# Kernel optimization log

Measured on AMD Instinct MI355X. Metric: run time of the kernel, lower is better.

The kernel has to match this reference:

```python
import jax, jax.numpy as jnp
import numpy as np


def setup_inputs() -> dict:
    key = jax.random.key(0)
    ks = jax.random.split(key, 5)
    B, C, T, Hh, Ww = 4, 64, 8, 32, 32
    HID = 32
    s = 0.05  # weight scale for numerically sane softmax logits
    return {
        "H": jax.random.normal(ks[0], (B, C, T, Hh, Ww), dtype=jnp.float32),
        "h": jax.random.normal(ks[1], (B, C, Hh, Ww), dtype=jnp.float32),
        "w_q": jax.random.normal(ks[2], (HID, C), dtype=jnp.float32) * s,
        "w_kv": jax.random.normal(ks[3], (HID, C), dtype=jnp.float32) * s,
        "w_o": jax.random.normal(ks[4], (C, HID), dtype=jnp.float32) * s,
    }


def reference(H, h, w_q, w_kv, w_o):
    B, C, T, Hh, Ww = H.shape
    N = Hh * Ww
    Hf = H.reshape(B, C, T, N)
    # 1x1 convs are pure channel-mixing matmuls
    H_kv = jnp.einsum('dc,bctn->bdtn', w_kv, Hf)                # [B, hid, T, N]
    h_q = jnp.einsum('dc,bchw->bdhw', w_q, h).reshape(B, -1, N)  # [B, hid, N]
    h_q = h_q.transpose(0, 2, 1)                                 # [B, N, hid]
    # per-timestep scores, vectorized over t: [B, T, N, N]
    a = jnp.einsum('bnd,bdtm->btnm', h_q, H_kv)
    # remove the diagonal of each per-timestep [N, N] block
    diag = jnp.einsum('btnn->btn', a)                            # [B, T, N]
    eye = jnp.eye(N, dtype=a.dtype)
    a = a - diag[..., :, None] * eye
    # concat over t along rows, softmax over the (T*N) row axis
    att = jax.nn.softmax(a.reshape(B, T * N, N), axis=1)         # [B, T*N, N]
    h_v = jnp.einsum('bdk,bkm->bdm', H_kv.reshape(B, -1, T * N), att)  # [B, hid, N]
    h_v = jnp.einsum('cd,bdhw->bchw', w_o, h_v.reshape(B, -1, Hh, Ww))
    return (h + h_v, att)
```

## Files before the change

### kernel.cpp

```cpp
#include <hip/hip_runtime.h>

typedef short bf16x8 __attribute__((ext_vector_type(8)));
typedef float f32x4  __attribute__((ext_vector_type(4)));
typedef unsigned short ushort_t;

#define HID 32
#define CC  64
#define TT  8
#define NN  1024
#define BB  4
#define KTOT 8192

__device__ __forceinline__ ushort_t f2b(float x) {
    unsigned int u = __float_as_uint(x);
    return (ushort_t)((u + 0x7fffu + ((u >> 16) & 1u)) >> 16);
}
__device__ __forceinline__ float b2f(ushort_t u) {
    return __uint_as_float((unsigned int)u << 16);
}

__global__ __launch_bounds__(256) void k_pre(const float* __restrict__ H,
                                             const float* __restrict__ h,
                                             const float* __restrict__ wq,
                                             const float* __restrict__ wkv,
                                             ushort_t* __restrict__ hqHI,
                                             ushort_t* __restrict__ hqLO,
                                             ushort_t* __restrict__ hkTH0,
                                             ushort_t* __restrict__ hkTH1,
                                             ushort_t* __restrict__ hkTL0,
                                             ushort_t* __restrict__ hkTL1,
                                             ushort_t* __restrict__ hkDB) {
    int bx = blockIdx.x;
    if (bx < 256) {
        int gid = bx * 256 + threadIdx.x;
        int dg = gid >> 15;
        int rest = gid & 32767;
        int b = rest >> 13, tn = rest & 8191;
        int d0 = dg << 4;
        float acc[16];
#pragma unroll
        for (int d = 0; d < 16; d++) acc[d] = 0.f;
        const float* Hb = H + (size_t)(b * CC) * KTOT + tn;
        const float* wb = wkv + d0 * CC;
#pragma unroll 8
        for (int c = 0; c < CC; c++) {
            float v = Hb[(size_t)c * KTOT];
#pragma unroll
            for (int d = 0; d < 16; d++) acc[d] += wb[d * CC + c] * v;
        }
        ushort_t thi[16], tlo[16];
#pragma unroll
        for (int d = 0; d < 16; d++) {
            ushort_t hi = f2b(acc[d]);
            thi[d] = hi;
            tlo[d] = f2b(acc[d] - b2f(hi));
        }
        size_t po = ((size_t)b * KTOT + tn) * 16;
        bf16x8* ohi = (bf16x8*)((dg ? hkTH1 : hkTH0) + po);
        bf16x8* olo = (bf16x8*)((dg ? hkTL1 : hkTL0) + po);
#pragma unroll
        for (int v8 = 0; v8 < 2; v8++) {
            bf16x8 a, l;
#pragma unroll
            for (int j = 0; j < 8; j++) { a[j] = (short)thi[v8*8+j]; l[j] = (short)tlo[v8*8+j]; }
            ohi[v8] = a; olo[v8] = l;
        }
#pragma unroll
        for (int d = 0; d < 16; d++)
            hkDB[((size_t)(b * HID) + d0 + d) * KTOT + tn] = thi[d];
    } else {
        int gid = (bx - 256) * 256 + threadIdx.x;
        int b = gid >> 10;
        float acc[HID];
#pragma unroll
        for (int d = 0; d < HID; d++) acc[d] = 0.f;
        const float* hb = h + (size_t)(b * CC) * NN + (gid & 1023);
#pragma unroll 4
        for (int c = 0; c < CC; c++) {
            float v = hb[c * NN];
#pragma unroll
            for (int d = 0; d < HID; d++) acc[d] += wq[d * CC + c] * v;
        }
        bf16x8* ohi = (bf16x8*)(hqHI + (size_t)gid * HID);
        bf16x8* olo = (bf16x8*)(hqLO + (size_t)gid * HID);
#pragma unroll
        for (int v8 = 0; v8 < 4; v8++) {
            bf16x8 thi, tlo;
#pragma unroll
            for (int j = 0; j < 8; j++) {
                float x = acc[v8 * 8 + j];
                ushort_t hi = f2b(x);
                thi[j] = (short)hi;
                tlo[j] = (short)f2b(x - b2f(hi));
            }
            ohi[v8] = thi; olo[v8] = tlo;
        }
    }
}

__global__ __launch_bounds__(1024) void k_fuse(const ushort_t* __restrict__ hqHI,
                                               const ushort_t* __restrict__ hqLO,
                                               const ushort_t* __restrict__ hkTH0,
                                               const ushort_t* __restrict__ hkTH1,
                                               const ushort_t* __restrict__ hkTL0,
                                               const ushort_t* __restrict__ hkTL1,
                                               const ushort_t* __restrict__ hkDB,
                                               const float* __restrict__ h,
                                               const float* __restrict__ wo,
                                               float* __restrict__ att,
                                               float* __restrict__ out0) {
    int bx = blockIdx.x;
    int logical = ((bx & 7) << 5) | (bx >> 3);
    int b = logical >> 6, mt = logical & 63;
    int mb = mt << 4;
    int tid = threadIdx.x;
    int wave = tid >> 6, lane = tid & 63;
    int g = lane >> 4, c = lane & 15;
    int t = wave >> 1;
    int nh = (wave & 1) << 9;

    __shared__ float csred[16][16];
    __shared__ float hvred[16][16][32];
    __shared__ float hvL[16][33];
    __shared__ __align__(16) ushort_t PT[16][16][40];

    size_t ako = ((size_t)b * KTOT + t * NN + (mb + c)) * 16 + (g & 1) * 8;
    bf16x8 akh = *(const bf16x8*)(((g >> 1) ? hkTH1 : hkTH0) + ako);
    bf16x8 akl = *(const bf16x8*)(((g >> 1) ? hkTL1 : hkTL0) + ako);

    const ushort_t* qhi = hqHI + ((size_t)(b << 10)) * HID;
    const ushort_t* qlo = hqLO + ((size_t)(b << 10)) * HID;
    const ushort_t* vb0 = hkDB + (size_t)(b * HID + c) * KTOT;
    const ushort_t* vb1 = hkDB + (size_t)(b * HID + 16 + c) * KTOT;
    ushort_t (*pt)[40] = PT[wave];

    f32x4 cs = {0.f, 0.f, 0.f, 0.f};
    f32x4 acc0 = {0.f,0.f,0.f,0.f}, acc1 = {0.f,0.f,0.f,0.f};
    for (int ks = 0; ks < 16; ks++) {
        int k0 = t * NN + nh + ks * 32;
#pragma unroll
        for (int half = 0; half < 2; half++) {
            int nb = nh + ks * 32 + half * 16;
            size_t qo = (size_t)(nb + c) * HID + 8 * g;
            bf16x8 qh = *(const bf16x8*)(qhi + qo);
            f32x4 sv = __builtin_amdgcn_mfma_f32_16x16x32_bf16(akh, qh, (f32x4){0.f,0.f,0.f,0.f}, 0, 0, 0);
            int n = nb + c;
            float e0 = __expf((n == mb + 4 * g + 0) ? 0.f : sv[0]);
            float e1 = __expf((n == mb + 4 * g + 1) ? 0.f : sv[1]);
            float e2 = __expf((n == mb + 4 * g + 2) ? 0.f : sv[2]);
            float e3 = __expf((n == mb + 4 * g + 3) ? 0.f : sv[3]);
            cs[0] += e0; cs[1] += e1; cs[2] += e2; cs[3] += e3;
            int kl = half * 16 + c;
            pt[4 * g + 0][kl] = f2b(e0);
            pt[4 * g + 1][kl] = f2b(e1);
            pt[4 * g + 2][kl] = f2b(e2);
            pt[4 * g + 3][kl] = f2b(e3);
        }
        bf16x8 pa = *(const bf16x8*)&pt[c][8 * g];
        bf16x8 v0 = *(const bf16x8*)(vb0 + k0 + 8 * g);
        bf16x8 v1 = *(const bf16x8*)(vb1 + k0 + 8 * g);
        acc0 = __builtin_amdgcn_mfma_f32_16x16x32_bf16(pa, v0, acc0, 0, 0, 0);
        acc1 = __builtin_amdgcn_mfma_f32_16x16x32_bf16(pa, v1, acc1, 0, 0, 0);
    }
#pragma unroll
    for (int off = 1; off <= 8; off <<= 1) {
        cs[0] += __shfl_xor(cs[0], off, 64);
        cs[1] += __shfl_xor(cs[1], off, 64);
        cs[2] += __shfl_xor(cs[2], off, 64);
        cs[3] += __shfl_xor(cs[3], off, 64);
    }
    if (c == 0) *(f32x4*)&csred[wave][4 * g] = cs;
    __syncthreads();
    f32x4 gs = {0.f, 0.f, 0.f, 0.f};
#pragma unroll
    for (int w = 0; w < 16; w++)
        gs += *(const f32x4*)&csred[w][4 * g];
    f32x4 vinv;
#pragma unroll
    for (int r = 0; r < 4; r++) vinv[r] = 1.0f / gs[r];

#pragma unroll
    for (int r = 0; r < 4; r++) {
        hvred[wave][4 * g + r][c]      = acc0[r] * vinv[r];
        hvred[wave][4 * g + r][16 + c] = acc1[r] * vinv[r];
    }

    float* attb = att + (size_t)b * KTOT * NN;
#pragma unroll 2
    for (int hs = 0; hs < 32; hs++) {
        int nb = nh + hs * 16;
        size_t qo = (size_t)(nb + c) * HID + 8 * g;
        bf16x8 qh = *(const bf16x8*)(qhi + qo);
        bf16x8 ql = *(const bf16x8*)(qlo + qo);
        f32x4 sv = __builtin_amdgcn_mfma_f32_16x16x32_bf16(akh, ql, (f32x4){0.f,0.f,0.f,0.f}, 0, 0, 0);
        sv = __builtin_amdgcn_mfma_f32_16x16x32_bf16(akl, qh, sv, 0, 0, 0);
        sv = __builtin_amdgcn_mfma_f32_16x16x32_bf16(akh, qh, sv, 0, 0, 0);
        int n = nb + c;
        f32x4 ev;
        ev[0] = __expf((n == mb + 4 * g + 0) ? 0.f : sv[0]) * vinv[0];
        ev[1] = __expf((n == mb + 4 * g + 1) ? 0.f : sv[1]) * vinv[1];
        ev[2] = __expf((n == mb + 4 * g + 2) ? 0.f : sv[2]) * vinv[2];
        ev[3] = __expf((n == mb + 4 * g + 3) ? 0.f : sv[3]) * vinv[3];
        *(f32x4*)(attb + (size_t)(t * NN + n) * NN + mb + 4 * g) = ev;
    }

    __syncthreads();
    if (tid < 512) {
        int m = tid >> 5, d = tid & 31;
        float s = 0.f;
#pragma unroll
        for (int w = 0; w < 16; w++) s += hvred[w][m][d];
        hvL[m][d] = s;
    }
    __syncthreads();
    {
        int cc = tid >> 4, mm = tid & 15;
        float v = h[(size_t)(b * CC + cc) * NN + mb + mm];
#pragma unroll
        for (int d = 0; d < HID; d++) v += wo[cc * HID + d] * hvL[mm][d];
        out0[(size_t)(b * CC + cc) * NN + mb + mm] = v;
    }
}

extern "C" void kernel_launch(void* const* d_in, const int* in_sizes, int n_in,
                              void* d_out, int out_size, void* d_ws, size_t ws_size,
                              hipStream_t stream) {
    const float* H   = (const float*)d_in[0];
    const float* h   = (const float*)d_in[1];
    const float* wq  = (const float*)d_in[2];
    const float* wkv = (const float*)d_in[3];
    const float* wo  = (const float*)d_in[4];

    float* out0 = (float*)d_out;
    float* att  = out0 + (size_t)BB * CC * NN;

    ushort_t* hqHI  = (ushort_t*)d_ws;
    ushort_t* hqLO  = hqHI  + 131072;
    ushort_t* hkTH0 = hqLO  + 131072;
    ushort_t* hkTH1 = hkTH0 + 524288;
    ushort_t* hkTL0 = hkTH1 + 524288;
    ushort_t* hkTL1 = hkTL0 + 524288;
    ushort_t* hkDB  = hkTL1 + 524288;

    k_pre <<<272, 256,  0, stream>>>(H, h, wq, wkv, hqHI, hqLO,
                                     hkTH0, hkTH1, hkTL0, hkTL1, hkDB);
    k_fuse<<<256, 1024, 0, stream>>>(hqHI, hqLO, hkTH0, hkTH1, hkTL0, hkTL1, hkDB,
                                     h, wo, att, out0);
}
```

Measured before the change: 85.10 us.

## Precompute softmax column sums in a separate kernel and fuse attention writes into main pass

Adds a k_psum kernel that computes partial softmax denominators over 32 K-chunks using the bf16-hi scores, so k_main can derive the normalizers up front. The main kernel then computes the exact 3-MFMA scores once, writing normalized attention and feeding the PV product in a single pass instead of two passes over N. This removes the recomputation of scores and the block-wide barrier before the attention write, at the cost of an extra launch and a separate sum pass. The normalizer now comes from hi-only scores while the numerators use the split-precision scores, so the rows may not sum exactly to one.

Result: no change. 85.62 us (+0.6%).

```diff
diff --git a/kernel.cpp b/kernel.cpp
--- a/kernel.cpp
+++ b/kernel.cpp
@@ -10,6 +10,8 @@
 #define NN  1024
 #define BB  4
 #define KTOT 8192
+#define NKC_P 32
+#define KCHUNK_P (KTOT/NKC_P)
 
 __device__ __forceinline__ ushort_t f2b(float x) {
     unsigned int u = __float_as_uint(x);
@@ -98,13 +100,56 @@
     }
 }
 
-__global__ __launch_bounds__(1024) void k_fuse(const ushort_t* __restrict__ hqHI,
+__global__ __launch_bounds__(512, 8) void k_psum(const ushort_t* __restrict__ hqHI,
+                                                 const ushort_t* __restrict__ hkTH0,
+                                                 const ushort_t* __restrict__ hkTH1,
+                                                 float* __restrict__ psum) {
+    int bx = blockIdx.x;
+    int b = bx >> 8, mt = (bx >> 5) & 7, kc = bx & 31;
+    int wave = threadIdx.x >> 6, lane = threadIdx.x & 63;
+    int g = lane >> 4, c = lane & 15;
+    int m = mt * 128 + wave * 16 + c;
+    int t = kc >> 2;
+    int nb0 = (kc & 3) << 8;
+
+    size_t bqo = ((size_t)b * KTOT + t * NN + m) * 16 + (g & 1) * 8;
+    bf16x8 bqh = *(const bf16x8*)(((g >> 1) ? hkTH1 : hkTH0) + bqo);
+
+    const ushort_t* qhi = hqHI + ((size_t)(b << 10)) * HID;
+
+    float csum0 = 0.f, csum1 = 0.f;
+    for (int s16 = 0; s16 < KCHUNK_P / 16; s16 += 2) {
+        int nbA = nb0 + s16 * 16;
+        int nbB = nbA + 16;
+        bf16x8 ahA = *(const bf16x8*)(qhi + (size_t)(nbA + c) * HID + 8 * g);
+        bf16x8 ahB = *(const bf16x8*)(qhi + (size_t)(nbB + c) * HID + 8 * g);
+        f32x4 svA = __builtin_amdgcn_mfma_f32_16x16x32_bf16(ahA, bqh, (f32x4){0.f,0.f,0.f,0.f}, 0, 0, 0);
+        f32x4 svB = __builtin_amdgcn_mfma_f32_16x16x32_bf16(ahB, bqh, (f32x4){0.f,0.f,0.f,0.f}, 0, 0, 0);
+        int nrowA = nbA + 4 * g;
+        int nrowB = nbB + 4 * g;
+#pragma unroll
+        for (int r = 0; r < 4; r++) {
+            float xA = (nrowA + r == m) ? 0.f : svA[r];
+            float xB = (nrowB + r == m) ? 0.f : svB[r];
+            csum0 += __expf(xA);
+            csum1 += __expf(xB);
+        }
+    }
+    float csum = csum0 + csum1;
+    csum += __shfl_xor(csum, 16);
+    csum += __shfl_xor(csum, 32);
+    if (lane < 16)
+        psum[(((size_t)(b * NKC_P + kc)) << 10) + mt * 128 + wave * 16 + lane] = csum;
+}
+
+__global__ __launch_bounds__(1024) void k_main(const ushort_t* __restrict__ hqHI,
                                                const ushort_t* __restrict__ hqLO,
                                                const ushort_t* __restrict__ hkTH0,
                                                const ushort_t* __restrict__ hkTH1,
                                                const ushort_t* __restrict__ hkTL0,
                                                const ushort_t* __restrict__ hkTL1,
                                                const ushort_t* __restrict__ hkDB,
+                                               const float* __restrict__ psum,
                                                const float* __restrict__ h,
                                                const float* __restrict__ wo,
                                                float* __restrict__ att,
@@ -119,10 +164,17 @@
     int t = wave >> 1;
     int nh = (wave & 1) << 9;
 
-    __shared__ float csred[16][16];
     __shared__ float hvred[16][16][32];
     __shared__ float hvL[16][33];
     __shared__ __align__(16) ushort_t PT[16][16][40];
+
+    f32x4 gs = {0.f, 0.f, 0.f, 0.f};
+#pragma unroll
+    for (int j = 0; j < NKC_P; j++)
+        gs += *(const f32x4*)(psum + (((size_t)(b * NKC_P + j)) << 10) + mb + 4 * g);
+    f32x4 vinv;
+#pragma unroll
+    for (int r = 0; r < 4; r++) vinv[r] = 1.0f / gs[r];
 
     size_t ako = ((size_t)b * KTOT + t * NN + (mb + c)) * 16 + (g & 1) * 8;
     bf16x8 akh = *(const bf16x8*)(((g >> 1) ? hkTH1 : hkTH0) + ako);
@@ -132,10 +184,11 @@
     const ushort_t* qlo = hqLO + ((size_t)(b << 10)) * HID;
     const ushort_t* vb0 = hkDB + (size_t)(b * HID + c) * KTOT;
     const ushort_t* vb1 = hkDB + (size_t)(b * HID + 16 + c) * KTOT;
+    float* attb = att + (size_t)b * KTOT * NN;
     ushort_t (*pt)[40] = PT[wave];
 
-    f32x4 cs = {0.f, 0.f, 0.f, 0.f};
     f32x4 acc0 = {0.f,0.f,0.f,0.f}, acc1 = {0.f,0.f,0.f,0.f};
+
     for (int ks = 0; ks < 16; ks++) {
         int k0 = t * NN + nh + ks * 32;
 #pragma unroll
@@ -143,13 +196,17 @@
             int nb = nh + ks * 32 + half * 16;
             size_t qo = (size_t)(nb + c) * HID + 8 * g;
             bf16x8 qh = *(const bf16x8*)(qhi + qo);
-            f32x4 sv = __builtin_amdgcn_mfma_f32_16x16x32_bf16(akh, qh, (f32x4){0.f,0.f,0.f,0.f}, 0, 0, 0);
+            bf16x8 ql = *(const bf16x8*)(qlo + qo);
+            f32x4 sv = __builtin_amdgcn_mfma_f32_16x16x32_bf16(akh, ql, (f32x4){0.f,0.f,0.f,0.f}, 0, 0, 0);
+            sv = __builtin_amdgcn_mfma_f32_16x16x32_bf16(akl, qh, sv, 0, 0, 0);
+            sv = __builtin_amdgcn_mfma_f32_16x16x32_bf16(akh, qh, sv, 0, 0, 0);
             int n = nb + c;
-            float e0 = __expf((n == mb + 4 * g + 0) ? 0.f : sv[0]);
-            float e1 = __expf((n == mb + 4 * g + 1) ? 0.f : sv[1]);
-            float e2 = __expf((n == mb + 4 * g + 2) ? 0.f : sv[2]);
-            float e3 = __expf((n == mb + 4 * g + 3) ? 0.f : sv[3]);
-            cs[0] += e0; cs[1] += e1; cs[2] += e2; cs[3] += e3;
+            float e0 = __expf((n == mb + 4 * g + 0) ? 0.f : sv[0]) * vinv[0];
+            float e1 = __expf((n == mb + 4 * g + 1) ? 0.f : sv[1]) * vinv[1];
+            float e2 = __expf((n == mb + 4 * g + 2) ? 0.f : sv[2]) * vinv[2];
+            float e3 = __expf((n == mb + 4 * g + 3) ? 0.f : sv[3]) * vinv[3];
+            f32x4 ev; ev[0] = e0; ev[1] = e1; ev[2] = e2; ev[3] = e3;
+            *(f32x4*)(attb + (size_t)(t * NN + n) * NN + mb + 4 * g) = ev;
             int kl = half * 16 + c;
             pt[4 * g + 0][kl] = f2b(e0);
             pt[4 * g + 1][kl] = f2b(e1);
@@ -162,48 +219,12 @@
         acc0 = __builtin_amdgcn_mfma_f32_16x16x32_bf16(pa, v0, acc0, 0, 0, 0);
         acc1 = __builtin_amdgcn_mfma_f32_16x16x32_bf16(pa, v1, acc1, 0, 0, 0);
     }
-#pragma unroll
-    for (int off = 1; off <= 8; off <<= 1) {
-        cs[0] += __shfl_xor(cs[0], off, 64);
-        cs[1] += __shfl_xor(cs[1], off, 64);
-        cs[2] += __shfl_xor(cs[2], off, 64);
-        cs[3] += __shfl_xor(cs[3], off, 64);
-    }
-    if (c == 0) *(f32x4*)&csred[wave][4 * g] = cs;
-    __syncthreads();
-    f32x4 gs = {0.f, 0.f, 0.f, 0.f};
-#pragma unroll
-    for (int w = 0; w < 16; w++)
-        gs += *(const f32x4*)&csred[w][4 * g];
-    f32x4 vinv;
-#pragma unroll
-    for (int r = 0; r < 4; r++) vinv[r] = 1.0f / gs[r];
 
 #pragma unroll
     for (int r = 0; r < 4; r++) {
-        hvred[wave][4 * g + r][c]      = acc0[r] * vinv[r];
-        hvred[wave][4 * g + r][16 + c] = acc1[r] * vinv[r];
-    }
-
-    float* attb = att + (size_t)b * KTOT * NN;
-#pragma unroll 2
-    for (int hs = 0; hs < 32; hs++) {
-        int nb = nh + hs * 16;
-        size_t qo = (size_t)(nb + c) * HID + 8 * g;
-        bf16x8 qh = *(const bf16x8*)(qhi + qo);
-        bf16x8 ql = *(const bf16x8*)(qlo + qo);
-        f32x4 sv = __builtin_amdgcn_mfma_f32_16x16x32_bf16(akh, ql, (f32x4){0.f,0.f,0.f,0.f}, 0, 0, 0);
-        sv = __builtin_amdgcn_mfma_f32_16x16x32_bf16(akl, qh, sv, 0, 0, 0);
-        sv = __builtin_amdgcn_mfma_f32_16x16x32_bf16(akh, qh, sv, 0, 0, 0);
-        int n = nb + c;
-        f32x4 ev;
-        ev[0] = __expf((n == mb + 4 * g + 0) ? 0.f : sv[0]) * vinv[0];
-        ev[1] = __expf((n == mb + 4 * g + 1) ? 0.f : sv[1]) * vinv[1];
-        ev[2] = __expf((n == mb + 4 * g + 2) ? 0.f : sv[2]) * vinv[2];
-        ev[3] = __expf((n == mb + 4 * g + 3) ? 0.f : sv[3]) * vinv[3];
-        *(f32x4*)(attb + (size_t)(t * NN + n) * NN + mb + 4 * g) = ev;
-    }
-
+        hvred[wave][4 * g + r][c]      = acc0[r];
+        hvred[wave][4 * g + r][16 + c] = acc1[r];
+    }
     __syncthreads();
     if (tid < 512) {
         int m = tid >> 5, d = tid & 31;
@@ -241,9 +262,11 @@
     ushort_t* hkTL0 = hkTH1 + 524288;
     ushort_t* hkTL1 = hkTL0 + 524288;
     ushort_t* hkDB  = hkTL1 + 524288;
-
-    k_pre <<<272, 256,  0, stream>>>(H, h, wq, wkv, hqHI, hqLO,
-                                     hkTH0, hkTH1, hkTL0, hkTL1, hkDB);
-    k_fuse<<<256, 1024, 0, stream>>>(hqHI, hqLO, hkTH0, hkTH1, hkTL0, hkTL1, hkDB,
-                                     h, wo, att, out0);
-}
+    float* psum = (float*)(hkDB + 1048576);
+
+    k_pre <<<272,  256,  0, stream>>>(H, h, wq, wkv, hqHI, hqLO,
+                                      hkTH0, hkTH1, hkTL0, hkTL1, hkDB);
+    k_psum<<<1024, 512,  0, stream>>>(hqHI, hkTH0, hkTH1, psum);
+    k_main<<<256,  1024, 0, stream>>>(hqHI, hqLO, hkTH0, hkTH1, hkTL0, hkTL1, hkDB,
+                                      psum, h, wo, att, out0);
+}
```

## Split attention-matrix write into separate kernel with row-contiguous tiling

Applied to the files above, without the earlier changes.

The fused kernel is split into two kernels. k_hv computes the column softmax sums and the output projection, and writes the per-column inverse sums to workspace. A new k_att kernel recomputes the scores and writes the attention matrix. k_att tiles each block over 64-column-wide stripes per wave across 128 rows, so stores cover full row segments and should coalesce better than the fused kernel's 16-column strips. This costs an extra kernel launch, a small workspace round trip, and recomputing the hi/lo score MFMAs.

New measurement: 83.82 us, median of 2. Within noise of the previous version (-1.5%).

```diff
diff --git a/kernel.cpp b/kernel.cpp
--- a/kernel.cpp
+++ b/kernel.cpp
@@ -98,17 +98,14 @@
     }
 }
 
-__global__ __launch_bounds__(1024) void k_fuse(const ushort_t* __restrict__ hqHI,
-                                               const ushort_t* __restrict__ hqLO,
-                                               const ushort_t* __restrict__ hkTH0,
-                                               const ushort_t* __restrict__ hkTH1,
-                                               const ushort_t* __restrict__ hkTL0,
-                                               const ushort_t* __restrict__ hkTL1,
-                                               const ushort_t* __restrict__ hkDB,
-                                               const float* __restrict__ h,
-                                               const float* __restrict__ wo,
-                                               float* __restrict__ att,
-                                               float* __restrict__ out0) {
+__global__ __launch_bounds__(1024) void k_hv(const ushort_t* __restrict__ hqHI,
+                                             const ushort_t* __restrict__ hkTH0,
+                                             const ushort_t* __restrict__ hkTH1,
+                                             const ushort_t* __restrict__ hkDB,
+                                             const float* __restrict__ h,
+                                             const float* __restrict__ wo,
+                                             float* __restrict__ inv,
+                                             float* __restrict__ out0) {
     int bx = blockIdx.x;
     int logical = ((bx & 7) << 5) | (bx >> 3);
     int b = logical >> 6, mt = logical & 63;
@@ -126,10 +123,8 @@
 
     size_t ako = ((size_t)b * KTOT + t * NN + (mb + c)) * 16 + (g & 1) * 8;
     bf16x8 akh = *(const bf16x8*)(((g >> 1) ? hkTH1 : hkTH0) + ako);
-    bf16x8 akl = *(const bf16x8*)(((g >> 1) ? hkTL1 : hkTL0) + ako);
 
     const ushort_t* qhi = hqHI + ((size_t)(b << 10)) * HID;
-    const ushort_t* qlo = hqLO + ((size_t)(b << 10)) * HID;
     const ushort_t* vb0 = hkDB + (size_t)(b * HID + c) * KTOT;
     const ushort_t* vb1 = hkDB + (size_t)(b * HID + 16 + c) * KTOT;
     ushort_t (*pt)[40] = PT[wave];
@@ -178,32 +173,14 @@
     f32x4 vinv;
 #pragma unroll
     for (int r = 0; r < 4; r++) vinv[r] = 1.0f / gs[r];
+    if (wave == 0 && c == 0)
+        *(f32x4*)(inv + (b << 10) + mb + 4 * g) = vinv;
 
 #pragma unroll
     for (int r = 0; r < 4; r++) {
         hvred[wave][4 * g + r][c]      = acc0[r] * vinv[r];
         hvred[wave][4 * g + r][16 + c] = acc1[r] * vinv[r];
     }
-
-    float* attb = att + (size_t)b * KTOT * NN;
-#pragma unroll 2
-    for (int hs = 0; hs < 32; hs++) {
-        int nb = nh + hs * 16;
-        size_t qo = (size_t)(nb + c) * HID + 8 * g;
-        bf16x8 qh = *(const bf16x8*)(qhi + qo);
-        bf16x8 ql = *(const bf16x8*)(qlo + qo);
-        f32x4 sv = __builtin_amdgcn_mfma_f32_16x16x32_bf16(akh, ql, (f32x4){0.f,0.f,0.f,0.f}, 0, 0, 0);
-        sv = __builtin_amdgcn_mfma_f32_16x16x32_bf16(akl, qh, sv, 0, 0, 0);
-        sv = __builtin_amdgcn_mfma_f32_16x16x32_bf16(akh, qh, sv, 0, 0, 0);
-        int n = nb + c;
-        f32x4 ev;
-        ev[0] = __expf((n == mb + 4 * g + 0) ? 0.f : sv[0]) * vinv[0];
-        ev[1] = __expf((n == mb + 4 * g + 1) ? 0.f : sv[1]) * vinv[1];
-        ev[2] = __expf((n == mb + 4 * g + 2) ? 0.f : sv[2]) * vinv[2];
-        ev[3] = __expf((n == mb + 4 * g + 3) ? 0.f : sv[3]) * vinv[3];
-        *(f32x4*)(attb + (size_t)(t * NN + n) * NN + mb + 4 * g) = ev;
-    }
-
     __syncthreads();
     if (tid < 512) {
         int m = tid >> 5, d = tid & 31;
@@ -219,6 +196,58 @@
 #pragma unroll
         for (int d = 0; d < HID; d++) v += wo[cc * HID + d] * hvL[mm][d];
         out0[(size_t)(b * CC + cc) * NN + mb + mm] = v;
+    }
+}
+
+__global__ __launch_bounds__(1024) void k_att(const ushort_t* __restrict__ hqHI,
+                                              const ushort_t* __restrict__ hqLO,
+                                              const ushort_t* __restrict__ hkTH0,
+                                              const ushort_t* __restrict__ hkTH1,
+                                              const ushort_t* __restrict__ hkTL0,
+                                              const ushort_t* __restrict__ hkTL1,
+                                              const float* __restrict__ inv,
+                                              float* __restrict__ att) {
+    int bx = blockIdx.x;
+    int b = bx >> 6, t = (bx >> 3) & 7, ng = bx & 7;
+    int tid = threadIdx.x;
+    int wave = tid >> 6, lane = tid & 63;
+    int g = lane >> 4, c = lane & 15;
+    int mf = wave << 6;
+
+    bf16x8 akh[4], akl[4];
+    f32x4 vinv[4];
+#pragma unroll
+    for (int f = 0; f < 4; f++) {
+        size_t ako = ((size_t)b * KTOT + t * NN + (mf + 16 * f + c)) * 16 + (g & 1) * 8;
+        akh[f] = *(const bf16x8*)(((g >> 1) ? hkTH1 : hkTH0) + ako);
+        akl[f] = *(const bf16x8*)(((g >> 1) ? hkTL1 : hkTL0) + ako);
+        vinv[f] = *(const f32x4*)(inv + (b << 10) + mf + 16 * f + 4 * g);
+    }
+
+    const ushort_t* qhi = hqHI + ((size_t)(b << 10)) * HID;
+    const ushort_t* qlo = hqLO + ((size_t)(b << 10)) * HID;
+    float* attb = att + (size_t)b * KTOT * NN;
+
+    for (int ks = 0; ks < 8; ks++) {
+        int nb = ng * 128 + ks * 16;
+        size_t qo = (size_t)(nb + c) * HID + 8 * g;
+        bf16x8 qh = *(const bf16x8*)(qhi + qo);
+        bf16x8 ql = *(const bf16x8*)(qlo + qo);
+        int n = nb + c;
+        float* rowp = attb + (size_t)(t * NN + n) * NN;
+#pragma unroll
+        for (int f = 0; f < 4; f++) {
+            f32x4 sv = __builtin_amdgcn_mfma_f32_16x16x32_bf16(akh[f], ql, (f32x4){0.f,0.f,0.f,0.f}, 0, 0, 0);
+            sv = __builtin_amdgcn_mfma_f32_16x16x32_bf16(akl[f], qh, sv, 0, 0, 0);
+            sv = __builtin_amdgcn_mfma_f32_16x16x32_bf16(akh[f], qh, sv, 0, 0, 0);
+            int mrow = mf + 16 * f + 4 * g;
+            f32x4 ev;
+            ev[0] = __expf((n == mrow + 0) ? 0.f : sv[0]) * vinv[f][0];
+            ev[1] = __expf((n == mrow + 1) ? 0.f : sv[1]) * vinv[f][1];
+            ev[2] = __expf((n == mrow + 2) ? 0.f : sv[2]) * vinv[f][2];
+            ev[3] = __expf((n == mrow + 3) ? 0.f : sv[3]) * vinv[f][3];
+            *(f32x4*)(rowp + mrow) = ev;
+        }
     }
 }
 
@@ -241,9 +270,10 @@
     ushort_t* hkTL0 = hkTH1 + 524288;
     ushort_t* hkTL1 = hkTL0 + 524288;
     ushort_t* hkDB  = hkTL1 + 524288;
-
-    k_pre <<<272, 256,  0, stream>>>(H, h, wq, wkv, hqHI, hqLO,
-                                     hkTH0, hkTH1, hkTL0, hkTL1, hkDB);
-    k_fuse<<<256, 1024, 0, stream>>>(hqHI, hqLO, hkTH0, hkTH1, hkTL0, hkTL1, hkDB,
-                                     h, wo, att, out0);
-}
+    float* inv  = (float*)(hkDB + 1048576);
+
+    k_pre<<<272, 256,  0, stream>>>(H, h, wq, wkv, hqHI, hqLO,
+                                    hkTH0, hkTH1, hkTL0, hkTL1, hkDB);
+    k_hv <<<256, 1024, 0, stream>>>(hqHI, hkTH0, hkTH1, hkDB, h, wo, inv, out0);
+    k_att<<<256, 1024, 0, stream>>>(hqHI, hqLO, hkTH0, hkTH1, hkTL0, hkTL1, inv, att);
+}
```
